# Kernel optimization log

Hardware: AMD Instinct MI355X
Metric: run time of the kernel (lower is better)

The kernel has to match this reference:

```python
import jax, jax.numpy as jnp
import numpy as np

BSZ, N, DEG = 32, 128, 8
HID, NODE_F, EDGE_F = 64, 32, 16
E_PER_G = N * DEG
E_TOT = BSZ * E_PER_G
N_TOT = BSZ * N


def _edges():
    # ring-style unique edges per graph: (i, (i+d) % N) for d in 1..DEG
    i = np.repeat(np.arange(N), DEG)              # [N*DEG]
    d = np.tile(np.arange(1, DEG + 1), N)
    src_l = np.tile(i, BSZ)                       # local src per edge
    dst_l = np.tile((i + d) % N, BSZ)
    off = np.repeat(np.arange(BSZ) * N, E_PER_G)
    ei = np.stack([src_l + off, dst_l + off])     # [2, E_TOT] global
    return jnp.asarray(ei, jnp.int32)


def setup_inputs() -> dict:
    key = jax.random.key(0)
    ks = jax.random.split(key, 16)
    def lin(k, fi, fo):
        s = 1.0 / np.sqrt(fi)
        kw, kb = jax.random.split(k)
        return (jax.random.uniform(kw, (fi, fo), jnp.float32, -s, s),
                jax.random.uniform(kb, (fo,), jnp.float32, -s, s))
    W_atom, b_atom = lin(ks[0], NODE_F, HID)
    W_bond, b_bond = lin(ks[1], EDGE_F, HID)
    be_w1, be_b1 = lin(ks[2], HID, HID)   # GINE bond_encoder MLP
    be_w2, be_b2 = lin(ks[3], HID, HID)
    nn_w1, nn_b1 = lin(ks[4], HID, HID)   # GINE update seq
    nn_w2, nn_b2 = lin(ks[5], HID, HID)
    m_w1, m_b1 = lin(ks[6], 2 * HID, HID) # final MLP: outer(HID)+edge(HID) -> HID -> 1
    m_w2, m_b2 = lin(ks[7], HID, 1)
    return {
        "x": jax.random.normal(ks[8], (N_TOT, NODE_F), jnp.float32),
        "edge_attr": jax.random.normal(ks[9], (E_TOT, EDGE_F), jnp.float32),
        "edge_index": _edges(),
        "batch": jnp.repeat(jnp.arange(BSZ, dtype=jnp.int32), N),
        "W_atom": W_atom, "b_atom": b_atom, "W_bond": W_bond, "b_bond": b_bond,
        "be_w1": be_w1, "be_b1": be_b1, "be_w2": be_w2, "be_b2": be_b2,
        "nn_w1": nn_w1, "nn_b1": nn_b1, "nn_w2": nn_w2, "nn_b2": nn_b2,
        "m_w1": m_w1, "m_b1": m_b1, "m_w2": m_w2, "m_b2": m_b2,
    }


def reference(x, edge_attr, edge_index, batch,
              W_atom, b_atom, W_bond, b_bond,
              be_w1, be_b1, be_w2, be_b2,
              nn_w1, nn_b1, nn_w2, nn_b2,
              m_w1, m_b1, m_w2, m_b2):
    src, dst = edge_index[0], edge_index[1]
    h = x @ W_atom + b_atom                                   # atom encoder [N_TOT, HID]
    e = edge_attr @ W_bond + b_bond                           # bond encoder [E_TOT, HID]
    # --- GINEConv (eps=0): nn(h + sum_j relu(h_j + mlp(e_ij))) ---
    ee = jax.nn.relu(e @ be_w1 + be_b1) @ be_w2 + be_b2
    msg = jax.nn.relu(h[src] + ee)
    agg = jax.ops.segment_sum(msg, dst, num_segments=N_TOT)
    h = jax.nn.relu((h + agg) @ nn_w1 + nn_b1) @ nn_w2 + nn_b2
    # --- dense batch (equal-size graphs -> exact reshape) ---
    logits = h.reshape(BSZ, N, HID)
    real_mask = jnp.ones((BSZ, N, N), dtype=bool)
    # --- outer pairwise tuples ---
    outer = jnp.einsum('bnk,bmk->bnmk', logits, logits)       # [B,N,N,HID]
    # --- scatter edge embeddings into dense [B,N,N,HID] ---
    g = src // N
    ls, ld = src % N, dst % N
    dense_e = jnp.zeros((BSZ, N, N, HID), e.dtype).at[g, ls, ld].set(e)
    emb = jnp.concatenate([outer, dense_e], axis=-1)          # [B,N,N,2*HID]
    emb = jax.nn.relu(emb @ m_w1 + m_b1) @ m_w2 + m_b2        # [B,N,N,1]
    return emb, real_mask
```

## Files before the change

kernel.cpp:

```cpp
#include <hip/hip_runtime.h>

#define BSZ 32
#define NN 128
#define DEG 8
#define HID 64
#define NODE_F 32
#define EDGE_F 16
#define E_PER_G (NN * DEG)
#define E_TOT (BSZ * E_PER_G)
#define N_TOT (BSZ * NN)
#define EMB_SIZE (BSZ * NN * NN)

typedef __attribute__((ext_vector_type(8))) short short8;
typedef __attribute__((ext_vector_type(4))) float f32x4;

__device__ __forceinline__ unsigned short f2bf(float f) {
    unsigned u = __builtin_bit_cast(unsigned, f);
    u += 0x7FFF + ((u >> 16) & 1);
    return (unsigned short)(u >> 16);
}
__device__ __forceinline__ float bf2f(unsigned short s) {
    unsigned u = ((unsigned)s) << 16;
    return __builtin_bit_cast(float, u);
}
__device__ __forceinline__ int lds_b(int row, int col) {
    return row * 128 + (((col >> 3) ^ (row & 7)) << 4) + ((col & 7) << 1);
}
__device__ __forceinline__ int lds_c(int row, int c8) {
    return row * 128 + ((c8 ^ (row & 7)) << 4);
}

__global__ __launch_bounds__(256) void k_atom(const float* __restrict__ x,
        const float* __restrict__ W, const float* __restrict__ b,
        float* __restrict__ h) {
    __shared__ float xs[16][NODE_F];
    int tid = threadIdx.x;
    {
        int i2 = tid * 2;
        float2 v = *(const float2*)&x[(size_t)blockIdx.x * 16 * NODE_F + i2];
        xs[i2 >> 5][i2 & 31] = v.x;
        xs[i2 >> 5][(i2 & 31) + 1] = v.y;
    }
    int j = tid & 63, q = tid >> 6;
    float ww[NODE_F];
#pragma unroll
    for (int k = 0; k < NODE_F; ++k) ww[k] = W[k * HID + j];
    float bj = b[j];
    __syncthreads();
#pragma unroll
    for (int r = 0; r < 4; ++r) {
        int row = q * 4 + r;
        float acc = bj;
#pragma unroll
        for (int k = 0; k < NODE_F; ++k) acc = fmaf(xs[row][k], ww[k], acc);
        h[(size_t)(blockIdx.x * 16 + row) * HID + j] = acc;
    }
}

__global__ void k_prep(const float* __restrict__ W_bond, const float* __restrict__ be_w1,
                       const float* __restrict__ be_w2, const float* __restrict__ m_w1,
                       const float* __restrict__ nn_w1, const float* __restrict__ nn_w2,
                       unsigned short* __restrict__ PK, unsigned short* __restrict__ W1T) {
    int t = blockIdx.x * 256 + threadIdx.x;
    int m = t >> 12;
    int idx = t & 4095;
    if (m < 6) {
        int i = idx & 7, lr = (idx >> 3) & 15, lg = (idx >> 7) & 3;
        int jt = (idx >> 9) & 3, kh = (idx >> 11) & 1;
        int k = kh * 32 + lg * 8 + i, j = jt * 16 + lr;
        float v;
        switch (m) {
            case 0:  v = (k < EDGE_F) ? W_bond[k * HID + j] : 0.f; break;
            case 1:  v = be_w1[k * HID + j]; break;
            case 2:  v = be_w2[k * HID + j]; break;
            case 3:  v = m_w1[(HID + k) * HID + j]; break;
            case 4:  v = nn_w1[k * HID + j]; break;
            default: v = nn_w2[k * HID + j]; break;
        }
        PK[m * 4096 + idx] = f2bf(v);
    } else {
        int j = idx >> 6, k = idx & 63;
        W1T[idx] = f2bf(m_w1[k * HID + j]);
    }
}

__global__ __launch_bounds__(256) void k_edgeM(
        const float* __restrict__ ea, const float* __restrict__ h,
        const float* __restrict__ b_bond, const float* __restrict__ be_b1,
        const float* __restrict__ be_b2, const unsigned short* __restrict__ PK,
        float* __restrict__ E1, unsigned short* __restrict__ msgb) {
    __shared__ char ebuf[128 * 128];
    __shared__ char tbuf[128 * 128];
    int tid = threadIdx.x;
    int w = tid >> 6, l = tid & 63, lr = l & 15, lg = l >> 4;
    int e0 = blockIdx.x * 128;
    int R0 = w * 32;

    short8 af[2];
#pragma unroll
    for (int mt = 0; mt < 2; ++mt) {
        short8 a = (short8){0, 0, 0, 0, 0, 0, 0, 0};
        if (lg < 2) {
            const float* p = ea + (size_t)(e0 + R0 + mt * 16 + lr) * EDGE_F + lg * 8;
            float4 x0 = *(const float4*)p;
            float4 x1 = *(const float4*)(p + 4);
            a[0] = (short)f2bf(x0.x); a[1] = (short)f2bf(x0.y);
            a[2] = (short)f2bf(x0.z); a[3] = (short)f2bf(x0.w);
            a[4] = (short)f2bf(x1.x); a[5] = (short)f2bf(x1.y);
            a[6] = (short)f2bf(x1.z); a[7] = (short)f2bf(x1.w);
        }
        af[mt] = a;
    }
    f32x4 a0[2][4];
#pragma unroll
    for (int mt = 0; mt < 2; ++mt)
#pragma unroll
        for (int jt = 0; jt < 4; ++jt) a0[mt][jt] = (f32x4){0.f, 0.f, 0.f, 0.f};
#pragma unroll
    for (int jt = 0; jt < 4; ++jt) {
        short8 bw = *(const short8*)(PK + 0 * 4096 + (size_t)(((0 * 4 + jt) * 4 + lg) * 16 + lr) * 8);
#pragma unroll
        for (int mt = 0; mt < 2; ++mt)
            a0[mt][jt] = __builtin_amdgcn_mfma_f32_16x16x32_bf16(af[mt], bw, a0[mt][jt], 0, 0, 0);
    }
    float bbv[4];
#pragma unroll
    for (int jt = 0; jt < 4; ++jt) bbv[jt] = b_bond[jt * 16 + lr];
#pragma unroll
    for (int mt = 0; mt < 2; ++mt)
#pragma unroll
        for (int jt = 0; jt < 4; ++jt)
#pragma unroll
            for (int r = 0; r < 4; ++r) {
                int row = R0 + mt * 16 + lg * 4 + r, col = jt * 16 + lr;
                *(unsigned short*)(ebuf + lds_b(row, col)) = f2bf(a0[mt][jt][r] + bbv[jt]);
            }
    short8 ae[2][2];
#pragma unroll
    for (int mt = 0; mt < 2; ++mt)
#pragma unroll
        for (int kh = 0; kh < 2; ++kh)
            ae[mt][kh] = *(const short8*)(ebuf + lds_c(R0 + mt * 16 + lr, kh * 4 + lg));
    f32x4 a1[2][4];
#pragma unroll
    for (int mt = 0; mt < 2; ++mt)
#pragma unroll
        for (int jt = 0; jt < 4; ++jt) a1[mt][jt] = (f32x4){0.f, 0.f, 0.f, 0.f};
#pragma unroll
    for (int kh = 0; kh < 2; ++kh)
#pragma unroll
        for (int jt = 0; jt < 4; ++jt) {
            short8 bw = *(const short8*)(PK + 3 * 4096 + (size_t)(((kh * 4 + jt) * 4 + lg) * 16 + lr) * 8);
#pragma unroll
            for (int mt = 0; mt < 2; ++mt)
                a1[mt][jt] = __builtin_amdgcn_mfma_f32_16x16x32_bf16(ae[mt][kh], bw, a1[mt][jt], 0, 0, 0);
        }
#pragma unroll
    for (int mt = 0; mt < 2; ++mt)
#pragma unroll
        for (int jt = 0; jt < 4; ++jt)
#pragma unroll
            for (int r = 0; r < 4; ++r)
                E1[(size_t)(e0 + R0 + mt * 16 + lg * 4 + r) * HID + jt * 16 + lr] = a1[mt][jt][r];
    float b1v[4];
#pragma unroll
    for (int jt = 0; jt < 4; ++jt) b1v[jt] = be_b1[jt * 16 + lr];
    f32x4 a2[2][4];
#pragma unroll
    for (int mt = 0; mt < 2; ++mt)
#pragma unroll
        for (int jt = 0; jt < 4; ++jt) a2[mt][jt] = (f32x4){0.f, 0.f, 0.f, 0.f};
#pragma unroll
    for (int kh = 0; kh < 2; ++kh)
#pragma unroll
        for (int jt = 0; jt < 4; ++jt) {
            short8 bw = *(const short8*)(PK + 1 * 4096 + (size_t)(((kh * 4 + jt) * 4 + lg) * 16 + lr) * 8);
#pragma unroll
            for (int mt = 0; mt < 2; ++mt)
                a2[mt][jt] = __builtin_amdgcn_mfma_f32_16x16x32_bf16(ae[mt][kh], bw, a2[mt][jt], 0, 0, 0);
        }
#pragma unroll
    for (int mt = 0; mt < 2; ++mt)
#pragma unroll
        for (int jt = 0; jt < 4; ++jt)
#pragma unroll
            for (int r = 0; r < 4; ++r) {
                int row = R0 + mt * 16 + lg * 4 + r, col = jt * 16 + lr;
                *(unsigned short*)(tbuf + lds_b(row, col)) = f2bf(fmaxf(a2[mt][jt][r] + b1v[jt], 0.f));
            }
    short8 at[2][2];
#pragma unroll
    for (int mt = 0; mt < 2; ++mt)
#pragma unroll
        for (int kh = 0; kh < 2; ++kh)
            at[mt][kh] = *(const short8*)(tbuf + lds_c(R0 + mt * 16 + lr, kh * 4 + lg));
    float b2v[4];
#pragma unroll
    for (int jt = 0; jt < 4; ++jt) b2v[jt] = be_b2[jt * 16 + lr];
    f32x4 a3[2][4];
#pragma unroll
    for (int mt = 0; mt < 2; ++mt)
#pragma unroll
        for (int jt = 0; jt < 4; ++jt) a3[mt][jt] = (f32x4){0.f, 0.f, 0.f, 0.f};
#pragma unroll
    for (int kh = 0; kh < 2; ++kh)
#pragma unroll
        for (int jt = 0; jt < 4; ++jt) {
            short8 bw = *(const short8*)(PK + 2 * 4096 + (size_t)(((kh * 4 + jt) * 4 + lg) * 16 + lr) * 8);
#pragma unroll
            for (int mt = 0; mt < 2; ++mt)
                a3[mt][jt] = __builtin_amdgcn_mfma_f32_16x16x32_bf16(at[mt][kh], bw, a3[mt][jt], 0, 0, 0);
        }
    int g = e0 >> 10;
#pragma unroll
    for (int mt = 0; mt < 2; ++mt)
#pragma unroll
        for (int jt = 0; jt < 4; ++jt)
#pragma unroll
            for (int r = 0; r < 4; ++r) {
                int row = R0 + mt * 16 + lg * 4 + r;
                int ig = (e0 & 1023) + row;
                int src = g * NN + (ig >> 3);
                float hv = h[(size_t)src * HID + jt * 16 + lr];
                float mv = fmaxf(hv + a3[mt][jt][r] + b2v[jt], 0.f);
                msgb[(size_t)(e0 + row) * HID + jt * 16 + lr] = f2bf(mv);
            }
}

__global__ __launch_bounds__(128) void k_nodeM(
        const float* __restrict__ h, const unsigned short* __restrict__ msgb,
        const float* __restrict__ nb1, const float* __restrict__ nb2,
        const unsigned short* __restrict__ PK, unsigned short* __restrict__ Lbf) {
    __shared__ char ub[16 * 128];
    __shared__ char tb[16 * 128];
    int tid = threadIdx.x;
    int n0 = blockIdx.x * 16;
    int g = n0 >> 7, nl0 = n0 & 127;
    {
        int r = tid >> 3;
        int c0 = (tid & 7) * 8;
        int nl = nl0 + r;
        float u[8];
        float4 h0 = *(const float4*)&h[(size_t)(n0 + r) * HID + c0];
        float4 h1 = *(const float4*)&h[(size_t)(n0 + r) * HID + c0 + 4];
        u[0] = h0.x; u[1] = h0.y; u[2] = h0.z; u[3] = h0.w;
        u[4] = h1.x; u[5] = h1.y; u[6] = h1.z; u[7] = h1.w;
#pragma unroll
        for (int d = 1; d <= 8; ++d) {
            int eid = g * E_PER_G + ((nl - d) & 127) * DEG + (d - 1);
            uint4 mv = *(const uint4*)&msgb[(size_t)eid * HID + c0];
            unsigned wd[4] = {mv.x, mv.y, mv.z, mv.w};
#pragma unroll
            for (int q = 0; q < 4; ++q) {
                u[q * 2]     += bf2f((unsigned short)(wd[q] & 0xffff));
                u[q * 2 + 1] += bf2f((unsigned short)(wd[q] >> 16));
            }
        }
        uint4 pk;
        pk.x = (unsigned)f2bf(u[0]) | ((unsigned)f2bf(u[1]) << 16);
        pk.y = (unsigned)f2bf(u[2]) | ((unsigned)f2bf(u[3]) << 16);
        pk.z = (unsigned)f2bf(u[4]) | ((unsigned)f2bf(u[5]) << 16);
        pk.w = (unsigned)f2bf(u[6]) | ((unsigned)f2bf(u[7]) << 16);
        *(uint4*)(ub + lds_c(r, tid & 7)) = pk;
    }
    __syncthreads();
    int w = tid >> 6, l = tid & 63, lr = l & 15, lg = l >> 4;
    short8 au[2];
#pragma unroll
    for (int kh = 0; kh < 2; ++kh)
        au[kh] = *(const short8*)(ub + lds_c(lr, kh * 4 + lg));
    f32x4 a1[2];
#pragma unroll
    for (int q = 0; q < 2; ++q) a1[q] = (f32x4){0.f, 0.f, 0.f, 0.f};
#pragma unroll
    for (int q = 0; q < 2; ++q) {
        int jt = w * 2 + q;
#pragma unroll
        for (int kh = 0; kh < 2; ++kh) {
            short8 bw = *(const short8*)(PK + 4 * 4096 + (size_t)(((kh * 4 + jt) * 4 + lg) * 16 + lr) * 8);
            a1[q] = __builtin_amdgcn_mfma_f32_16x16x32_bf16(au[kh], bw, a1[q], 0, 0, 0);
        }
    }
#pragma unroll
    for (int q = 0; q < 2; ++q) {
        int jt = w * 2 + q;
        float b1j = nb1[jt * 16 + lr];
#pragma unroll
        for (int r = 0; r < 4; ++r) {
            int row = lg * 4 + r, col = jt * 16 + lr;
            *(unsigned short*)(tb + lds_b(row, col)) = f2bf(fmaxf(a1[q][r] + b1j, 0.f));
        }
    }
    __syncthreads();
    short8 at[2];
#pragma unroll
    for (int kh = 0; kh < 2; ++kh)
        at[kh] = *(const short8*)(tb + lds_c(lr, kh * 4 + lg));
    f32x4 a2[2];
#pragma unroll
    for (int q = 0; q < 2; ++q) a2[q] = (f32x4){0.f, 0.f, 0.f, 0.f};
#pragma unroll
    for (int q = 0; q < 2; ++q) {
        int jt = w * 2 + q;
#pragma unroll
        for (int kh = 0; kh < 2; ++kh) {
            short8 bw = *(const short8*)(PK + 5 * 4096 + (size_t)(((kh * 4 + jt) * 4 + lg) * 16 + lr) * 8);
            a2[q] = __builtin_amdgcn_mfma_f32_16x16x32_bf16(at[kh], bw, a2[q], 0, 0, 0);
        }
    }
#pragma unroll
    for (int q = 0; q < 2; ++q) {
        int jt = w * 2 + q;
        float b2j = nb2[jt * 16 + lr];
#pragma unroll
        for (int r = 0; r < 4; ++r) {
            int row = lg * 4 + r;
            Lbf[(size_t)(n0 + row) * HID + jt * 16 + lr] = f2bf(a2[q][r] + b2j);
        }
    }
}

__global__ __launch_bounds__(512, 2) void k_pair(
        const unsigned short* __restrict__ Lbf, const float* __restrict__ E1,
        const unsigned short* __restrict__ W1T,
        const float* __restrict__ m_b1, const float* __restrict__ m_w2,
        const float* __restrict__ m_b2, float* __restrict__ out,
        float* __restrict__ mask, int write_mask) {
    __shared__ uint4 Ls[1024];
    int tid = threadIdx.x;
    int b = blockIdx.x >> 5;
    int nb = (blockIdx.x & 31) * 4;
    if (write_mask && tid < 128) {
        *(float4*)(mask + (size_t)(b * NN + nb) * NN + tid * 4) =
            make_float4(1.f, 1.f, 1.f, 1.f);
    }
    const uint4* src = (const uint4*)(Lbf + (size_t)b * NN * HID);
#pragma unroll
    for (int it = 0; it < 2; ++it) {
        int i = it * 512 + tid;
        int row = i >> 3, c = i & 7;
        Ls[(row << 3) | (c ^ (row & 7))] = src[i];
    }
    __syncthreads();
    int w = tid >> 6, l = tid & 63, lr = l & 15, lg = l >> 4;
    int n = nb + (w >> 1);
    int hm = (w & 1) * 64;
    const unsigned short* Lsu = (const unsigned short*)Ls;

    short8 w1t[2][4];
#pragma unroll
    for (int kh = 0; kh < 2; ++kh)
#pragma unroll
        for (int jt = 0; jt < 4; ++jt)
            w1t[kh][jt] = *(const short8*)(W1T + (size_t)(jt * 16 + lr) * HID + kh * 32 + lg * 8);
    short8 lnc[2];
#pragma unroll
    for (int kh = 0; kh < 2; ++kh) {
        int c = kh * 4 + lg;
        lnc[kh] = *(const short8*)(Lsu + (size_t)((n << 3) | (c ^ (n & 7))) * 8);
    }
    short8 an[2][4];
#pragma unroll
    for (int kh = 0; kh < 2; ++kh) {
        float lf[8];
#pragma unroll
        for (int i = 0; i < 8; ++i) lf[i] = bf2f((unsigned short)lnc[kh][i]);
#pragma unroll
        for (int jt = 0; jt < 4; ++jt)
#pragma unroll
            for (int i = 0; i < 8; ++i)
                an[kh][jt][i] = (short)f2bf(lf[i] * bf2f((unsigned short)w1t[kh][jt][i]));
    }

    f32x4 acc[4][4];
#pragma unroll
    for (int mt = 0; mt < 4; ++mt)
#pragma unroll
        for (int jt = 0; jt < 4; ++jt)
            acc[mt][jt] = (f32x4){0.f, 0.f, 0.f, 0.f};
#pragma unroll
    for (int mt = 0; mt < 4; ++mt) {
        int row = hm + mt * 16 + lr;
#pragma unroll
        for (int kh = 0; kh < 2; ++kh) {
            int c = kh * 4 + lg;
            short8 afr = *(const short8*)(Lsu + (size_t)((row << 3) | (c ^ (row & 7))) * 8);
#pragma unroll
            for (int jt = 0; jt < 4; ++jt)
                acc[mt][jt] = __builtin_amdgcn_mfma_f32_16x16x32_bf16(an[kh][jt], afr, acc[mt][jt], 0, 0, 0);
        }
    }
    float4 b1v[4], w2v[4];
#pragma unroll
    for (int jt = 0; jt < 4; ++jt) {
        b1v[jt] = *(const float4*)&m_b1[jt * 16 + lg * 4];
        w2v[jt] = *(const float4*)&m_w2[jt * 16 + lg * 4];
    }
    float bias2 = m_b2[0];
    float* orow = out + ((size_t)(b * NN + n)) * NN;
#pragma unroll
    for (int mt = 0; mt < 4; ++mt) {
        int m = hm + mt * 16 + lr;
        int d = (m - n) & 127;
        bool has_e = (unsigned)(d - 1) < 8u;
        float s = 0.f;
        if (has_e) {
            const float* ep = E1 + (size_t)(b * E_PER_G + n * DEG + (d - 1)) * HID;
#pragma unroll
            for (int jt = 0; jt < 4; ++jt) {
                float4 e1 = *(const float4*)&ep[jt * 16 + lg * 4];
                s = fmaf(fmaxf(acc[mt][jt][0] + b1v[jt].x + e1.x, 0.f), w2v[jt].x, s);
                s = fmaf(fmaxf(acc[mt][jt][1] + b1v[jt].y + e1.y, 0.f), w2v[jt].y, s);
                s = fmaf(fmaxf(acc[mt][jt][2] + b1v[jt].z + e1.z, 0.f), w2v[jt].z, s);
                s = fmaf(fmaxf(acc[mt][jt][3] + b1v[jt].w + e1.w, 0.f), w2v[jt].w, s);
            }
        } else {
#pragma unroll
            for (int jt = 0; jt < 4; ++jt) {
                s = fmaf(fmaxf(acc[mt][jt][0] + b1v[jt].x, 0.f), w2v[jt].x, s);
                s = fmaf(fmaxf(acc[mt][jt][1] + b1v[jt].y, 0.f), w2v[jt].y, s);
                s = fmaf(fmaxf(acc[mt][jt][2] + b1v[jt].z, 0.f), w2v[jt].z, s);
                s = fmaf(fmaxf(acc[mt][jt][3] + b1v[jt].w, 0.f), w2v[jt].w, s);
            }
        }
        s += __shfl_xor(s, 16);
        s += __shfl_xor(s, 32);
        if (lg == 0) orow[m] = s + bias2;
    }
}

extern "C" void kernel_launch(void* const* d_in, const int* in_sizes, int n_in,
                              void* d_out, int out_size, void* d_ws, size_t ws_size,
                              hipStream_t stream) {
    const float* x         = (const float*)d_in[0];
    const float* edge_attr = (const float*)d_in[1];
    const float* W_atom = (const float*)d_in[4];
    const float* b_atom = (const float*)d_in[5];
    const float* W_bond = (const float*)d_in[6];
    const float* b_bond = (const float*)d_in[7];
    const float* be_w1  = (const float*)d_in[8];
    const float* be_b1  = (const float*)d_in[9];
    const float* be_w2  = (const float*)d_in[10];
    const float* be_b2  = (const float*)d_in[11];
    const float* nn_w1  = (const float*)d_in[12];
    const float* nn_b1  = (const float*)d_in[13];
    const float* nn_w2  = (const float*)d_in[14];
    const float* nn_b2  = (const float*)d_in[15];
    const float* m_w1   = (const float*)d_in[16];
    const float* m_b1   = (const float*)d_in[17];
    const float* m_w2   = (const float*)d_in[18];
    const float* m_b2   = (const float*)d_in[19];

    char* ws = (char*)d_ws;
    float* h   = (float*)ws;                   ws += (size_t)N_TOT * HID * 4;
    float* E1  = (float*)ws;                   ws += (size_t)E_TOT * HID * 4;
    unsigned short* msgb = (unsigned short*)ws; ws += (size_t)E_TOT * HID * 2;
    unsigned short* Lbf  = (unsigned short*)ws; ws += (size_t)N_TOT * HID * 2;
    unsigned short* W1T  = (unsigned short*)ws; ws += (size_t)HID * HID * 2;
    unsigned short* PK   = (unsigned short*)ws; ws += (size_t)6 * 4096 * 2;

    k_atom<<<N_TOT / 16, 256, 0, stream>>>(x, W_atom, b_atom, h);
    k_prep<<<7 * 4096 / 256, 256, 0, stream>>>(W_bond, be_w1, be_w2, m_w1,
                                               nn_w1, nn_w2, PK, W1T);
    k_edgeM<<<E_TOT / 128, 256, 0, stream>>>(edge_attr, h, b_bond, be_b1, be_b2,
                                             PK, E1, msgb);
    k_nodeM<<<N_TOT / 16, 128, 0, stream>>>(h, msgb, nn_b1, nn_b2, PK, Lbf);

    float* out = (float*)d_out;
    float* mask = out + EMB_SIZE;
    int write_mask = (out_size >= 2 * EMB_SIZE) ? 1 : 0;
    k_pair<<<BSZ * 32, 512, 0, stream>>>(Lbf, E1, W1T, m_b1, m_w2, m_b2,
                                         out, mask, write_mask);
}
```

Measured before the change: 48.16 us.

## Merge atom/prep kernels, halve edge block size, stage edge embeddings in LDS

Fuses the atom encoder and weight-packing kernels into one launch by splitting the grid between the two jobs, saving one kernel launch. Halves the edge-MLP block to 64 edges with 128 threads, doubling the block count for better occupancy and load balance. In the pair kernel, the block's contiguous E1 segment is preloaded into shared memory, and the accumulators are restructured per m-tile to lower register pressure. The risks are extra LDS use, which could limit occupancy, and a __syncthreads inside a block-uniform branch of the fused kernel.

```diff
diff --git a/kernel.cpp b/kernel.cpp
--- a/kernel.cpp
+++ b/kernel.cpp
@@ -30,70 +30,69 @@
     return row * 128 + ((c8 ^ (row & 7)) << 4);
 }
 
-__global__ __launch_bounds__(256) void k_atom(const float* __restrict__ x,
-        const float* __restrict__ W, const float* __restrict__ b,
-        float* __restrict__ h) {
-    __shared__ float xs[16][NODE_F];
+__global__ __launch_bounds__(256) void k_pre(const float* __restrict__ x,
+        const float* __restrict__ W_atom, const float* __restrict__ b_atom,
+        const float* __restrict__ W_bond, const float* __restrict__ be_w1,
+        const float* __restrict__ be_w2, const float* __restrict__ m_w1,
+        const float* __restrict__ nn_w1, const float* __restrict__ nn_w2,
+        float* __restrict__ h, unsigned short* __restrict__ PK,
+        unsigned short* __restrict__ W1T) {
     int tid = threadIdx.x;
-    {
+    if (blockIdx.x < 256) {
+        __shared__ float xs[16][NODE_F];
         int i2 = tid * 2;
         float2 v = *(const float2*)&x[(size_t)blockIdx.x * 16 * NODE_F + i2];
         xs[i2 >> 5][i2 & 31] = v.x;
         xs[i2 >> 5][(i2 & 31) + 1] = v.y;
-    }
-    int j = tid & 63, q = tid >> 6;
-    float ww[NODE_F];
-#pragma unroll
-    for (int k = 0; k < NODE_F; ++k) ww[k] = W[k * HID + j];
-    float bj = b[j];
-    __syncthreads();
-#pragma unroll
-    for (int r = 0; r < 4; ++r) {
-        int row = q * 4 + r;
-        float acc = bj;
-#pragma unroll
-        for (int k = 0; k < NODE_F; ++k) acc = fmaf(xs[row][k], ww[k], acc);
-        h[(size_t)(blockIdx.x * 16 + row) * HID + j] = acc;
-    }
-}
-
-__global__ void k_prep(const float* __restrict__ W_bond, const float* __restrict__ be_w1,
-                       const float* __restrict__ be_w2, const float* __restrict__ m_w1,
-                       const float* __restrict__ nn_w1, const float* __restrict__ nn_w2,
-                       unsigned short* __restrict__ PK, unsigned short* __restrict__ W1T) {
-    int t = blockIdx.x * 256 + threadIdx.x;
-    int m = t >> 12;
-    int idx = t & 4095;
-    if (m < 6) {
-        int i = idx & 7, lr = (idx >> 3) & 15, lg = (idx >> 7) & 3;
-        int jt = (idx >> 9) & 3, kh = (idx >> 11) & 1;
-        int k = kh * 32 + lg * 8 + i, j = jt * 16 + lr;
-        float v;
-        switch (m) {
-            case 0:  v = (k < EDGE_F) ? W_bond[k * HID + j] : 0.f; break;
-            case 1:  v = be_w1[k * HID + j]; break;
-            case 2:  v = be_w2[k * HID + j]; break;
-            case 3:  v = m_w1[(HID + k) * HID + j]; break;
-            case 4:  v = nn_w1[k * HID + j]; break;
-            default: v = nn_w2[k * HID + j]; break;
-        }
-        PK[m * 4096 + idx] = f2bf(v);
+        int j = tid & 63, q = tid >> 6;
+        float ww[NODE_F];
+#pragma unroll
+        for (int k = 0; k < NODE_F; ++k) ww[k] = W_atom[k * HID + j];
+        float bj = b_atom[j];
+        __syncthreads();
+#pragma unroll
+        for (int r = 0; r < 4; ++r) {
+            int row = q * 4 + r;
+            float acc = bj;
+#pragma unroll
+            for (int k = 0; k < NODE_F; ++k) acc = fmaf(xs[row][k], ww[k], acc);
+            h[(size_t)(blockIdx.x * 16 + row) * HID + j] = acc;
+        }
     } else {
-        int j = idx >> 6, k = idx & 63;
-        W1T[idx] = f2bf(m_w1[k * HID + j]);
-    }
-}
-
-__global__ __launch_bounds__(256) void k_edgeM(
+        int t = (blockIdx.x - 256) * 256 + tid;
+        int m = t >> 12;
+        int idx = t & 4095;
+        if (m < 6) {
+            int i = idx & 7, lr = (idx >> 3) & 15, lg = (idx >> 7) & 3;
+            int jt = (idx >> 9) & 3, kh = (idx >> 11) & 1;
+            int k = kh * 32 + lg * 8 + i, j = jt * 16 + lr;
+            float v;
+            switch (m) {
+                case 0:  v = (k < EDGE_F) ? W_bond[k * HID + j] : 0.f; break;
+                case 1:  v = be_w1[k * HID + j]; break;
+                case 2:  v = be_w2[k * HID + j]; break;
+                case 3:  v = m_w1[(HID + k) * HID + j]; break;
+                case 4:  v = nn_w1[k * HID + j]; break;
+                default: v = nn_w2[k * HID + j]; break;
+            }
+            PK[m * 4096 + idx] = f2bf(v);
+        } else {
+            int j = idx >> 6, k = idx & 63;
+            W1T[idx] = f2bf(m_w1[k * HID + j]);
+        }
+    }
+}
+
+__global__ __launch_bounds__(128) void k_edgeM(
         const float* __restrict__ ea, const float* __restrict__ h,
         const float* __restrict__ b_bond, const float* __restrict__ be_b1,
         const float* __restrict__ be_b2, const unsigned short* __restrict__ PK,
         float* __restrict__ E1, unsigned short* __restrict__ msgb) {
-    __shared__ char ebuf[128 * 128];
-    __shared__ char tbuf[128 * 128];
+    __shared__ char ebuf[64 * 128];
+    __shared__ char tbuf[64 * 128];
     int tid = threadIdx.x;
     int w = tid >> 6, l = tid & 63, lr = l & 15, lg = l >> 4;
-    int e0 = blockIdx.x * 128;
+    int e0 = blockIdx.x * 64;
     int R0 = w * 32;
 
     short8 af[2];
@@ -327,6 +326,7 @@
         const float* __restrict__ m_b2, float* __restrict__ out,
         float* __restrict__ mask, int write_mask) {
     __shared__ uint4 Ls[1024];
+    __shared__ float eseg[4][8][64];
     int tid = threadIdx.x;
     int b = blockIdx.x >> 5;
     int nb = (blockIdx.x & 31) * 4;
@@ -341,86 +341,78 @@
         int row = i >> 3, c = i & 7;
         Ls[(row << 3) | (c ^ (row & 7))] = src[i];
     }
+    {
+        const float* ep = E1 + (size_t)(b * E_PER_G + nb * DEG) * HID;
+        ((float4*)&eseg[0][0][0])[tid] = ((const float4*)ep)[tid];
+    }
     __syncthreads();
     int w = tid >> 6, l = tid & 63, lr = l & 15, lg = l >> 4;
     int n = nb + (w >> 1);
     int hm = (w & 1) * 64;
     const unsigned short* Lsu = (const unsigned short*)Ls;
 
-    short8 w1t[2][4];
-#pragma unroll
-    for (int kh = 0; kh < 2; ++kh)
-#pragma unroll
-        for (int jt = 0; jt < 4; ++jt)
-            w1t[kh][jt] = *(const short8*)(W1T + (size_t)(jt * 16 + lr) * HID + kh * 32 + lg * 8);
-    short8 lnc[2];
+    short8 an[2][4];
 #pragma unroll
     for (int kh = 0; kh < 2; ++kh) {
         int c = kh * 4 + lg;
-        lnc[kh] = *(const short8*)(Lsu + (size_t)((n << 3) | (c ^ (n & 7))) * 8);
-    }
-    short8 an[2][4];
-#pragma unroll
-    for (int kh = 0; kh < 2; ++kh) {
+        short8 lnc = *(const short8*)(Lsu + (size_t)((n << 3) | (c ^ (n & 7))) * 8);
         float lf[8];
 #pragma unroll
-        for (int i = 0; i < 8; ++i) lf[i] = bf2f((unsigned short)lnc[kh][i]);
-#pragma unroll
-        for (int jt = 0; jt < 4; ++jt)
+        for (int i = 0; i < 8; ++i) lf[i] = bf2f((unsigned short)lnc[i]);
+#pragma unroll
+        for (int jt = 0; jt < 4; ++jt) {
+            short8 w1t = *(const short8*)(W1T + (size_t)(jt * 16 + lr) * HID + kh * 32 + lg * 8);
 #pragma unroll
             for (int i = 0; i < 8; ++i)
-                an[kh][jt][i] = (short)f2bf(lf[i] * bf2f((unsigned short)w1t[kh][jt][i]));
-    }
-
-    f32x4 acc[4][4];
-#pragma unroll
-    for (int mt = 0; mt < 4; ++mt)
-#pragma unroll
-        for (int jt = 0; jt < 4; ++jt)
-            acc[mt][jt] = (f32x4){0.f, 0.f, 0.f, 0.f};
+                an[kh][jt][i] = (short)f2bf(lf[i] * bf2f((unsigned short)w1t[i]));
+        }
+    }
+
+    float4 b1v[4], w2v[4];
+#pragma unroll
+    for (int jt = 0; jt < 4; ++jt) {
+        b1v[jt] = *(const float4*)&m_b1[jt * 16 + lg * 4];
+        w2v[jt] = *(const float4*)&m_w2[jt * 16 + lg * 4];
+    }
+    float bias2 = m_b2[0];
+    float* orow = out + ((size_t)(b * NN + n)) * NN;
+    const float* es = &eseg[w >> 1][0][0];
+
 #pragma unroll
     for (int mt = 0; mt < 4; ++mt) {
         int row = hm + mt * 16 + lr;
+        f32x4 acc[4];
+#pragma unroll
+        for (int jt = 0; jt < 4; ++jt) acc[jt] = (f32x4){0.f, 0.f, 0.f, 0.f};
 #pragma unroll
         for (int kh = 0; kh < 2; ++kh) {
             int c = kh * 4 + lg;
             short8 afr = *(const short8*)(Lsu + (size_t)((row << 3) | (c ^ (row & 7))) * 8);
 #pragma unroll
             for (int jt = 0; jt < 4; ++jt)
-                acc[mt][jt] = __builtin_amdgcn_mfma_f32_16x16x32_bf16(an[kh][jt], afr, acc[mt][jt], 0, 0, 0);
-        }
-    }
-    float4 b1v[4], w2v[4];
-#pragma unroll
-    for (int jt = 0; jt < 4; ++jt) {
-        b1v[jt] = *(const float4*)&m_b1[jt * 16 + lg * 4];
-        w2v[jt] = *(const float4*)&m_w2[jt * 16 + lg * 4];
-    }
-    float bias2 = m_b2[0];
-    float* orow = out + ((size_t)(b * NN + n)) * NN;
-#pragma unroll
-    for (int mt = 0; mt < 4; ++mt) {
-        int m = hm + mt * 16 + lr;
+                acc[jt] = __builtin_amdgcn_mfma_f32_16x16x32_bf16(an[kh][jt], afr, acc[jt], 0, 0, 0);
+        }
+        int m = row;
         int d = (m - n) & 127;
         bool has_e = (unsigned)(d - 1) < 8u;
         float s = 0.f;
         if (has_e) {
-            const float* ep = E1 + (size_t)(b * E_PER_G + n * DEG + (d - 1)) * HID;
+            const float* ep = es + (d - 1) * HID;
 #pragma unroll
             for (int jt = 0; jt < 4; ++jt) {
                 float4 e1 = *(const float4*)&ep[jt * 16 + lg * 4];
-                s = fmaf(fmaxf(acc[mt][jt][0] + b1v[jt].x + e1.x, 0.f), w2v[jt].x, s);
-                s = fmaf(fmaxf(acc[mt][jt][1] + b1v[jt].y + e1.y, 0.f), w2v[jt].y, s);
-                s = fmaf(fmaxf(acc[mt][jt][2] + b1v[jt].z + e1.z, 0.f), w2v[jt].z, s);
-                s = fmaf(fmaxf(acc[mt][jt][3] + b1v[jt].w + e1.w, 0.f), w2v[jt].w, s);
+                s = fmaf(fmaxf(acc[jt][0] + b1v[jt].x + e1.x, 0.f), w2v[jt].x, s);
+                s = fmaf(fmaxf(acc[jt][1] + b1v[jt].y + e1.y, 0.f), w2v[jt].y, s);
+                s = fmaf(fmaxf(acc[jt][2] + b1v[jt].z + e1.z, 0.f), w2v[jt].z, s);
+                s = fmaf(fmaxf(acc[jt][3] + b1v[jt].w + e1.w, 0.f), w2v[jt].w, s);
             }
         } else {
 #pragma unroll
             for (int jt = 0; jt < 4; ++jt) {
-                s = fmaf(fmaxf(acc[mt][jt][0] + b1v[jt].x, 0.f), w2v[jt].x, s);
-                s = fmaf(fmaxf(acc[mt][jt][1] + b1v[jt].y, 0.f), w2v[jt].y, s);
-                s = fmaf(fmaxf(acc[mt][jt][2] + b1v[jt].z, 0.f), w2v[jt].z, s);
-                s = fmaf(fmaxf(acc[mt][jt][3] + b1v[jt].w, 0.f), w2v[jt].w, s);
+                s = fmaf(fmaxf(acc[jt][0] + b1v[jt].x, 0.f), w2v[jt].x, s);
+                s = fmaf(fmaxf(acc[jt][1] + b1v[jt].y, 0.f), w2v[jt].y, s);
+                s = fmaf(fmaxf(acc[jt][2] + b1v[jt].z, 0.f), w2v[jt].z, s);
+                s = fmaf(fmaxf(acc[jt][3] + b1v[jt].w, 0.f), w2v[jt].w, s);
             }
         }
         s += __shfl_xor(s, 16);
@@ -459,11 +451,10 @@
     unsigned short* W1T  = (unsigned short*)ws; ws += (size_t)HID * HID * 2;
     unsigned short* PK   = (unsigned short*)ws; ws += (size_t)6 * 4096 * 2;
 
-    k_atom<<<N_TOT / 16, 256, 0, stream>>>(x, W_atom, b_atom, h);
-    k_prep<<<7 * 4096 / 256, 256, 0, stream>>>(W_bond, be_w1, be_w2, m_w1,
-                                               nn_w1, nn_w2, PK, W1T);
-    k_edgeM<<<E_TOT / 128, 256, 0, stream>>>(edge_attr, h, b_bond, be_b1, be_b2,
-                                             PK, E1, msgb);
+    k_pre<<<256 + 112, 256, 0, stream>>>(x, W_atom, b_atom, W_bond, be_w1, be_w2,
+                                         m_w1, nn_w1, nn_w2, h, PK, W1T);
+    k_edgeM<<<E_TOT / 64, 128, 0, stream>>>(edge_attr, h, b_bond, be_b1, be_b2,
+                                            PK, E1, msgb);
     k_nodeM<<<N_TOT / 16, 128, 0, stream>>>(h, msgb, nn_b1, nn_b2, PK, Lbf);
 
     float* out = (float*)d_out;
```

Measured after the change: 50.55 us. 4.9% more time.
